# Kernel optimization log

Measured on AMD Instinct MI355X. Metric: run time of the kernel, lower is better.

## Reference

```python
import jax, jax.numpy as jnp
import numpy as np

HIDDEN = 1024

def setup_inputs() -> dict:
    key = jax.random.key(0)
    ks = jax.random.split(key, 7)
    s = 1.0 / np.sqrt(HIDDEN)
    X = jax.random.normal(ks[0], (4, 2048, HIDDEN), dtype=jnp.float32)
    Wq = jax.random.uniform(ks[1], (HIDDEN, HIDDEN), jnp.float32, -s, s)
    bq = jax.random.uniform(ks[2], (HIDDEN,), jnp.float32, -s, s)
    Wk = jax.random.uniform(ks[3], (HIDDEN, HIDDEN), jnp.float32, -s, s)
    bk = jax.random.uniform(ks[4], (HIDDEN,), jnp.float32, -s, s)
    Wv = jax.random.uniform(ks[5], (HIDDEN, HIDDEN), jnp.float32, -s, s)
    bv = jax.random.uniform(ks[6], (HIDDEN,), jnp.float32, -s, s)
    return {"X": X, "Wq": Wq, "bq": bq, "Wk": Wk, "bk": bk, "Wv": Wv, "bv": bv}

def reference(X, Wq, bq, Wk, bk, Wv, bv):
    # torch Linear: x @ W.T + b
    q = jnp.einsum('bsd,ed->bse', X, Wq) + bq  # [B,S,H]
    k = jnp.einsum('bsd,ed->bse', X, Wk) + bk
    v = jnp.einsum('bsd,ed->bse', X, Wv) + bv
    scores = jnp.einsum('bqd,bkd->bqk', q, k) / jnp.sqrt(jnp.float32(HIDDEN))  # [B,S,S]
    attn = jax.nn.softmax(scores, axis=-1)
    return jnp.einsum('bqk,bkd->bqd', attn, v)
```

## Files before the change

### kernel.cpp

```cpp
#include <hip/hip_runtime.h>
#include <hip/hip_bf16.h>
#include <stdint.h>

#define B_ 4
#define S_ 2048
#define H_ 1024

typedef __attribute__((ext_vector_type(4))) float f32x4;
typedef __attribute__((ext_vector_type(8))) short bf16x8;

#define AS1C(p) ((const __attribute__((address_space(1))) void*)(p))
#define AS3(p)  ((__attribute__((address_space(3))) void*)(p))

__global__ __launch_bounds__(256)
void prep_k(const float* __restrict__ X,
            const float* __restrict__ Wq, const float* __restrict__ Wk,
            const float* __restrict__ Wv,
            const float* __restrict__ bq, const float* __restrict__ bk,
            const float* __restrict__ bv,
            __hip_bfloat16* __restrict__ Xb, __hip_bfloat16* __restrict__ Wall,
            float* __restrict__ ball, float* __restrict__ rsum)
{
    const int NX = B_ * S_ * H_ / 4;
    const int NW = H_ * H_ / 4;
    int i = blockIdx.x * blockDim.x + threadIdx.x;
    if (i < NX + 3 * NW) {
        const float* src; uint64_t* dst; int li;
        if (i < NX) { src = X; dst = (uint64_t*)Xb; li = i; }
        else {
            int j = i - NX;
            int wsel = j / NW; li = j - wsel * NW;
            src = (wsel == 0) ? Wq : (wsel == 1) ? Wk : Wv;
            dst = (uint64_t*)Wall + (size_t)wsel * NW;
        }
        float4 v = ((const float4*)src)[li];
        union { __hip_bfloat16 h[4]; uint64_t u; } o;
        o.h[0] = __float2bfloat16(v.x);
        o.h[1] = __float2bfloat16(v.y);
        o.h[2] = __float2bfloat16(v.z);
        o.h[3] = __float2bfloat16(v.w);
        dst[li] = o.u;
    } else {
        int j = i - (NX + 3 * NW);
        if (j < 3 * H_ / 4) {
            int bsel = j >> 8;
            int off  = j & 255;
            const float* src = (bsel == 0) ? bq : (bsel == 1) ? bk : bv;
            ((float4*)ball)[j] = ((const float4*)src)[off];
        } else if (j < 3 * H_ / 4 + B_ * S_ / 4) {
            int j2 = j - 3 * H_ / 4;
            ((float4*)rsum)[j2] = make_float4(0.f, 0.f, 0.f, 0.f);
        }
    }
}

template<int BN, bool OUT_BF16, bool EXP_SUM, bool ROWDIV>
__global__ __launch_bounds__(512, 2)
void gemm2ph(const __hip_bfloat16* __restrict__ A, int lda, long long aBatch,
             const __hip_bfloat16* __restrict__ B, int ldb, long long bBatch,
             void* __restrict__ Cout, int ldc, long long cBatch,
             float* __restrict__ rsum, int K, float scale)
{
    constexpr int FJ = BN / 64;
    constexpr int GB = BN / 64;
    __shared__ __hip_bfloat16 lA[2 * 256 * 64];
    __shared__ __hip_bfloat16 lB[2 * BN * 64];

    const int t  = threadIdx.x;
    const int bz = blockIdx.z;
    A += (long long)bz * aBatch;
    B += (long long)bz * bBatch;
    const int bm = blockIdx.y * 256;
    const int bn = blockIdx.x * BN;

    const int wave = t >> 6;
    const int lane = t & 63;
    const int wm = (wave >> 2) * 128;
    const int wn = (wave & 3) * (BN / 4);
    const int lm = lane & 15;
    const int kq = lane >> 4;
    const int cro = lm & 7;

    const int srow = t >> 3;
    const int swz  = ((t & 7) ^ (srow & 7)) * 8;
    const __hip_bfloat16* gA = A + (long long)(bm + srow) * lda + swz;
    const __hip_bfloat16* gB = B + (long long)(bn + srow) * ldb + swz;

    f32x4 acc[8][FJ] = {};

    auto stage = [&](int buf, int k0) {
        __hip_bfloat16* dA = lA + buf * (256 * 64) + t * 8;
        __hip_bfloat16* dB = lB + buf * (BN * 64) + t * 8;
#pragma unroll
        for (int g = 0; g < 4; ++g)
            __builtin_amdgcn_global_load_lds(AS1C(gA + (long long)g * 64 * lda + k0),
                                             AS3(dA + g * 4096), 16, 0, 0);
#pragma unroll
        for (int g = 0; g < GB; ++g)
            __builtin_amdgcn_global_load_lds(AS1C(gB + (long long)g * 64 * ldb + k0),
                                             AS3(dB + g * 4096), 16, 0, 0);
    };

    stage(0, 0);
    __syncthreads();

    const int nT = K >> 6;
    int buf = 0;
    for (int tt = 0; tt < nT; ++tt) {
        if (tt + 1 < nT) stage(buf ^ 1, (tt + 1) * 64);
        const __hip_bfloat16* cA = lA + buf * (256 * 64) + (wm + lm) * 64;
        const __hip_bfloat16* cB = lB + buf * (BN * 64) + (wn + lm) * 64;
#pragma unroll
        for (int ks = 0; ks < 2; ++ks) {
            const int ch = ((ks * 4 + kq) ^ cro) * 8;
            bf16x8 af[8], bfr[FJ];
#pragma unroll
            for (int i = 0; i < 8; ++i)
                af[i] = *(const bf16x8*)(cA + i * 16 * 64 + ch);
#pragma unroll
            for (int j = 0; j < FJ; ++j)
                bfr[j] = *(const bf16x8*)(cB + j * 16 * 64 + ch);
#pragma unroll
            for (int i = 0; i < 8; ++i)
#pragma unroll
                for (int j = 0; j < FJ; ++j)
                    acc[i][j] = __builtin_amdgcn_mfma_f32_16x16x32_bf16(
                        af[i], bfr[j], acc[i][j], 0, 0, 0);
        }
        __syncthreads();
        buf ^= 1;
    }

    if (EXP_SUM) {
#pragma unroll
        for (int fi = 0; fi < 8; ++fi) {
            const int rowb = bm + wm + fi * 16 + kq * 4;
            float ps[4] = {0.f, 0.f, 0.f, 0.f};
#pragma unroll
            for (int nj = 0; nj < FJ; ++nj) {
                const int col = bn + wn + nj * 16 + lm;
#pragma unroll
                for (int r = 0; r < 4; ++r) {
                    float e = __expf(acc[fi][nj][r] * scale);
                    ps[r] += e;
                    ((__hip_bfloat16*)Cout)[(long long)bz * cBatch +
                        (long long)(rowb + r) * ldc + col] = __float2bfloat16(e);
                }
            }
#pragma unroll
            for (int r = 0; r < 4; ++r) {
#pragma unroll
                for (int m = 1; m < 16; m <<= 1)
                    ps[r] += __shfl_xor(ps[r], m);
            }
            if (lm == 0) {
#pragma unroll
                for (int r = 0; r < 4; ++r)
                    atomicAdd(rsum + bz * S_ + rowb + r, ps[r]);
            }
        }
        return;
    }

#pragma unroll
    for (int fi = 0; fi < 8; ++fi) {
        const int rowb = bm + wm + fi * 16 + kq * 4;
        float inv[4];
        if (ROWDIV) {
            float4 rs = *(const float4*)(rsum + bz * S_ + rowb);
            inv[0] = 1.0f / rs.x; inv[1] = 1.0f / rs.y;
            inv[2] = 1.0f / rs.z; inv[3] = 1.0f / rs.w;
        }
#pragma unroll
        for (int nj = 0; nj < FJ; ++nj) {
            const int col = bn + wn + nj * 16 + lm;
#pragma unroll
            for (int r = 0; r < 4; ++r) {
                float val = ROWDIV ? acc[fi][nj][r] * inv[r] : acc[fi][nj][r] * scale;
                long long idx = (long long)bz * cBatch + (long long)(rowb + r) * ldc + col;
                if (OUT_BF16) ((__hip_bfloat16*)Cout)[idx] = __float2bfloat16(val);
                else          ((float*)Cout)[idx] = val;
            }
        }
    }
}

template<int BN, int MINW, bool OUT_BF16, bool HAS_BIAS, bool V_SPLIT, bool EXP_SUM, bool ROWDIV>
__global__ __launch_bounds__(256, MINW)
void gemm_bt(const __hip_bfloat16* __restrict__ A, int lda, long long aBatch,
             const __hip_bfloat16* __restrict__ B, int ldb, long long bBatch,
             const float* __restrict__ bias,
             void* __restrict__ Cout, int ldc, long long cBatch,
             __hip_bfloat16* __restrict__ vtrans, float* __restrict__ rsum,
             int M, int N, int K, float scale)
{
    constexpr int FJ = BN / 32;
    constexpr int SN = BN / 32;
    __shared__ __hip_bfloat16 lA[128 * 64];
    __shared__ __hip_bfloat16 lB[BN * 64];

    const int t  = threadIdx.x;
    const int bz = blockIdx.z;
    A += (long long)bz * aBatch;
    B += (long long)bz * bBatch;
    const int bm = blockIdx.y * 128;
    const int bn = blockIdx.x * BN;

    const int wave = t >> 6;
    const int lane = t & 63;
    const int wm = (wave & 1) * 64;
    const int wn = (wave >> 1) * (BN / 2);
    const int lm = lane & 15;
    const int kq = lane >> 4;
    const int cro = lm & 7;

    f32x4 acc[4][FJ] = {};

    const int srow = t >> 3;
    const int swz  = ((t & 7) ^ ((t >> 3) & 7)) * 8;
    const __hip_bfloat16* gA = A + (long long)(bm + srow) * lda + swz;
    const __hip_bfloat16* gB = B + (long long)(bn + srow) * ldb + swz;
    __hip_bfloat16* sA = lA + t * 8;
    __hip_bfloat16* sB = lB + t * 8;

    for (int k0 = 0; k0 < K; k0 += 64) {
        __syncthreads();
#pragma unroll
        for (int s = 0; s < 4; ++s)
            __builtin_amdgcn_global_load_lds(AS1C(gA + (long long)s * 32 * lda + k0),
                                             AS3(sA + s * 2048), 16, 0, 0);
#pragma unroll
        for (int s = 0; s < SN; ++s)
            __builtin_amdgcn_global_load_lds(AS1C(gB + (long long)s * 32 * ldb + k0),
                                             AS3(sB + s * 2048), 16, 0, 0);
        __syncthreads();

#pragma unroll
        for (int ks = 0; ks < 2; ++ks) {
            bf16x8 af[4], bfr[FJ];
            const int ch = ((ks * 4 + kq) ^ cro) * 8;
#pragma unroll
            for (int i = 0; i < 4; ++i)
                af[i] = *(const bf16x8*)(lA + (wm + i * 16 + lm) * 64 + ch);
#pragma unroll
            for (int j = 0; j < FJ; ++j)
                bfr[j] = *(const bf16x8*)(lB + (wn + j * 16 + lm) * 64 + ch);
#pragma unroll
            for (int i = 0; i < 4; ++i)
#pragma unroll
                for (int j = 0; j < FJ; ++j)
                    acc[i][j] = __builtin_amdgcn_mfma_f32_16x16x32_bf16(af[i], bfr[j], acc[i][j], 0, 0, 0);
        }
    }

    const bool vmode = V_SPLIT && (bn >= 2 * H_);
    const int r0q = kq * 4;

    if (EXP_SUM) {
#pragma unroll
        for (int i = 0; i < 4; ++i) {
            const int rowb = bm + wm + i * 16 + r0q;
            float ps[4] = {0.f, 0.f, 0.f, 0.f};
#pragma unroll
            for (int j = 0; j < FJ; ++j) {
                const int col = bn + wn + j * 16 + lm;
#pragma unroll
                for (int r = 0; r < 4; ++r) {
                    float e = __expf(acc[i][j][r] * scale);
                    ps[r] += e;
                    ((__hip_bfloat16*)Cout)[(long long)bz * cBatch +
                        (long long)(rowb + r) * ldc + col] = __float2bfloat16(e);
                }
            }
#pragma unroll
            for (int r = 0; r < 4; ++r) {
#pragma unroll
                for (int m = 1; m < 16; m <<= 1)
                    ps[r] += __shfl_xor(ps[r], m);
            }
            if (lm == 0) {
#pragma unroll
                for (int r = 0; r < 4; ++r)
                    atomicAdd(rsum + bz * S_ + rowb + r, ps[r]);
            }
        }
        return;
    }

#pragma unroll
    for (int i = 0; i < 4; ++i) {
        const int rowb = bm + wm + i * 16 + r0q;
        float inv[4];
        if (ROWDIV) {
            float4 rs = *(const float4*)(rsum + bz * S_ + rowb);
            inv[0] = 1.0f / rs.x; inv[1] = 1.0f / rs.y;
            inv[2] = 1.0f / rs.z; inv[3] = 1.0f / rs.w;
        }
#pragma unroll
        for (int j = 0; j < FJ; ++j) {
            const int col = bn + wn + j * 16 + lm;
            float bvv = 0.0f;
            if (HAS_BIAS) bvv = bias[col];
            if (!vmode) {
#pragma unroll
                for (int r = 0; r < 4; ++r) {
                    float val = ROWDIV ? acc[i][j][r] * inv[r]
                                       : acc[i][j][r] * scale + bvv;
                    long long idx = (long long)bz * cBatch + (long long)(rowb + r) * ldc + col;
                    if (OUT_BF16) ((__hip_bfloat16*)Cout)[idx] = __float2bfloat16(val);
                    else          ((float*)Cout)[idx] = val;
                }
            } else {
                const long long ebase = (long long)((rowb >> 11) * H_ + col - 2 * H_) * S_;
                union { ushort4 u; __hip_bfloat16 h[4]; } o;
#pragma unroll
                for (int r = 0; r < 4; ++r)
                    o.h[r] = __float2bfloat16(acc[i][j][r] + bvv);
                *(ushort4*)(vtrans + ebase + (rowb & 2047)) = o.u;
            }
        }
    }
}

extern "C" void kernel_launch(void* const* d_in, const int* in_sizes, int n_in,
                              void* d_out, int out_size, void* d_ws, size_t ws_size,
                              hipStream_t stream)
{
    const float* X  = (const float*)d_in[0];
    const float* Wq = (const float*)d_in[1];
    const float* bq = (const float*)d_in[2];
    const float* Wk = (const float*)d_in[3];
    const float* bk = (const float*)d_in[4];
    const float* Wv = (const float*)d_in[5];
    const float* bv = (const float*)d_in[6];
    float* out = (float*)d_out;

    char* w = (char*)d_ws;
    const size_t MB = 1ull << 20;
    __hip_bfloat16* Xb   = (__hip_bfloat16*)(w + 0);
    __hip_bfloat16* Wall = (__hip_bfloat16*)(w + 16 * MB);
    float*          ball = (float*)        (w + 22 * MB);
    __hip_bfloat16* sc   = (__hip_bfloat16*)(w + 0);
    __hip_bfloat16* qk   = (__hip_bfloat16*)(w + 32 * MB);
    __hip_bfloat16* vtb  = (__hip_bfloat16*)(w + 64 * MB);
    float*          rsum = (float*)        (w + 80 * MB);

    const int prep_items = B_ * S_ * H_ / 4 + 3 * H_ * H_ / 4 + 3 * H_ / 4 + B_ * S_ / 4;
    prep_k<<<(prep_items + 255) / 256, 256, 0, stream>>>(X, Wq, Wk, Wv, bq, bk, bv,
                                                         Xb, Wall, ball, rsum);

    dim3 g1(3 * H_ / 128, (B_ * S_) / 128, 1);
    gemm_bt<128, 1, true, true, true, false, false><<<g1, 256, 0, stream>>>(
        Xb, H_, 0, Wall, H_, 0, ball, qk, 2 * H_, 0, vtb, nullptr,
        B_ * S_, 3 * H_, H_, 1.0f);

    dim3 g2(S_ / 256, S_ / 256, B_);
    gemm2ph<256, true, true, false><<<g2, 512, 0, stream>>>(
        qk,      2 * H_, (long long)S_ * 2 * H_,
        qk + H_, 2 * H_, (long long)S_ * 2 * H_,
        sc, S_, (long long)S_ * S_, rsum, H_, 0.03125f);

    dim3 g3(H_ / 128, S_ / 256, B_);
    gemm2ph<128, false, false, true><<<g3, 512, 0, stream>>>(
        sc,  S_, (long long)S_ * S_,
        vtb, S_, (long long)H_ * S_,
        out, H_, (long long)S_ * H_, rsum, S_, 1.0f);
}
```

Before: 253.0 us.

## Replace two-phase GEMM with 8-phase ping-pong pipelined 256x256 tile kernel

Replaces the double-buffered gemm2ph kernel with gemm8p, which splits each 64-wide K step into four quadrant sub-steps. Barriers, sched_barriers, explicit vmcnt waits and s_setprio interleave LDS fragment loads, async global-to-LDS staging and MFMA bursts. The PV GEMM moves from 256x128 to 256x256 tiles at one block per CU, which halves its grid, and the prep kernel becomes a grid-stride loop with a fixed 2048-block launch. The aim is better overlap of memory and MFMA, at the cost of many more barriers and lower occupancy.

```diff
diff --git a/kernel.cpp b/kernel.cpp
--- a/kernel.cpp
+++ b/kernel.cpp
@@ -11,6 +11,9 @@
 
 #define AS1C(p) ((const __attribute__((address_space(1))) void*)(p))
 #define AS3(p)  ((__attribute__((address_space(3))) void*)(p))
+#define BAR()     __builtin_amdgcn_s_barrier()
+#define SCHED0()  __builtin_amdgcn_sched_barrier(0)
+#define WAITVM(n) asm volatile("s_waitcnt vmcnt(" #n ")" ::: "memory")
 
 __global__ __launch_bounds__(256)
 void prep_k(const float* __restrict__ X,
@@ -23,125 +26,160 @@
 {
     const int NX = B_ * S_ * H_ / 4;
     const int NW = H_ * H_ / 4;
-    int i = blockIdx.x * blockDim.x + threadIdx.x;
-    if (i < NX + 3 * NW) {
-        const float* src; uint64_t* dst; int li;
-        if (i < NX) { src = X; dst = (uint64_t*)Xb; li = i; }
-        else {
-            int j = i - NX;
-            int wsel = j / NW; li = j - wsel * NW;
-            src = (wsel == 0) ? Wq : (wsel == 1) ? Wk : Wv;
-            dst = (uint64_t*)Wall + (size_t)wsel * NW;
-        }
-        float4 v = ((const float4*)src)[li];
-        union { __hip_bfloat16 h[4]; uint64_t u; } o;
-        o.h[0] = __float2bfloat16(v.x);
-        o.h[1] = __float2bfloat16(v.y);
-        o.h[2] = __float2bfloat16(v.z);
-        o.h[3] = __float2bfloat16(v.w);
-        dst[li] = o.u;
-    } else {
-        int j = i - (NX + 3 * NW);
-        if (j < 3 * H_ / 4) {
-            int bsel = j >> 8;
-            int off  = j & 255;
-            const float* src = (bsel == 0) ? bq : (bsel == 1) ? bk : bv;
-            ((float4*)ball)[j] = ((const float4*)src)[off];
-        } else if (j < 3 * H_ / 4 + B_ * S_ / 4) {
-            int j2 = j - 3 * H_ / 4;
-            ((float4*)rsum)[j2] = make_float4(0.f, 0.f, 0.f, 0.f);
+    const int TOT = NX + 3 * NW + 3 * H_ / 4 + B_ * S_ / 4;
+    const int stride = gridDim.x * blockDim.x;
+    for (int i = blockIdx.x * blockDim.x + threadIdx.x; i < TOT; i += stride) {
+        if (i < NX + 3 * NW) {
+            const float* src; uint64_t* dst; int li;
+            if (i < NX) { src = X; dst = (uint64_t*)Xb; li = i; }
+            else {
+                int j = i - NX;
+                int wsel = j / NW; li = j - wsel * NW;
+                src = (wsel == 0) ? Wq : (wsel == 1) ? Wk : Wv;
+                dst = (uint64_t*)Wall + (size_t)wsel * NW;
+            }
+            float4 v = ((const float4*)src)[li];
+            union { __hip_bfloat16 h[4]; uint64_t u; } o;
+            o.h[0] = __float2bfloat16(v.x);
+            o.h[1] = __float2bfloat16(v.y);
+            o.h[2] = __float2bfloat16(v.z);
+            o.h[3] = __float2bfloat16(v.w);
+            dst[li] = o.u;
+        } else {
+            int j = i - (NX + 3 * NW);
+            if (j < 3 * H_ / 4) {
+                int bsel = j >> 8;
+                int off  = j & 255;
+                const float* src = (bsel == 0) ? bq : (bsel == 1) ? bk : bv;
+                ((float4*)ball)[j] = ((const float4*)src)[off];
+            } else {
+                int j2 = j - 3 * H_ / 4;
+                ((float4*)rsum)[j2] = make_float4(0.f, 0.f, 0.f, 0.f);
+            }
         }
     }
 }
 
-template<int BN, bool OUT_BF16, bool EXP_SUM, bool ROWDIV>
-__global__ __launch_bounds__(512, 2)
-void gemm2ph(const __hip_bfloat16* __restrict__ A, int lda, long long aBatch,
-             const __hip_bfloat16* __restrict__ B, int ldb, long long bBatch,
-             void* __restrict__ Cout, int ldc, long long cBatch,
-             float* __restrict__ rsum, int K, float scale)
+template<bool EXP_SUM, bool ROWDIV, bool OUT_BF16>
+__global__ __launch_bounds__(512, 1)
+void gemm8p(const __hip_bfloat16* __restrict__ A, int lda, long long aBatch,
+            const __hip_bfloat16* __restrict__ B, int ldb, long long bBatch,
+            void* __restrict__ Cout, int ldc, long long cBatch,
+            float* __restrict__ rsum, int K, float scale)
 {
-    constexpr int FJ = BN / 64;
-    constexpr int GB = BN / 64;
-    __shared__ __hip_bfloat16 lA[2 * 256 * 64];
-    __shared__ __hip_bfloat16 lB[2 * BN * 64];
+    __shared__ __hip_bfloat16 lA[2][2][128 * 64];
+    __shared__ __hip_bfloat16 lB[2][2][128 * 64];
 
     const int t  = threadIdx.x;
     const int bz = blockIdx.z;
     A += (long long)bz * aBatch;
     B += (long long)bz * bBatch;
     const int bm = blockIdx.y * 256;
-    const int bn = blockIdx.x * BN;
-
-    const int wave = t >> 6;
-    const int lane = t & 63;
-    const int wm = (wave >> 2) * 128;
-    const int wn = (wave & 3) * (BN / 4);
-    const int lm = lane & 15;
-    const int kq = lane >> 4;
+    const int bn = blockIdx.x * 256;
+
+    const int wave = t >> 6, lane = t & 63;
+    const int wm2 = (wave >> 2) * 64;
+    const int wn2 = (wave & 3) * 32;
+    const int lm = lane & 15, kq = lane >> 4;
     const int cro = lm & 7;
 
+    f32x4 acc[8][4] = {};
+
     const int srow = t >> 3;
-    const int swz  = ((t & 7) ^ (srow & 7)) * 8;
-    const __hip_bfloat16* gA = A + (long long)(bm + srow) * lda + swz;
-    const __hip_bfloat16* gB = B + (long long)(bn + srow) * ldb + swz;
-
-    f32x4 acc[8][FJ] = {};
-
-    auto stage = [&](int buf, int k0) {
-        __hip_bfloat16* dA = lA + buf * (256 * 64) + t * 8;
-        __hip_bfloat16* dB = lB + buf * (BN * 64) + t * 8;
-#pragma unroll
-        for (int g = 0; g < 4; ++g)
-            __builtin_amdgcn_global_load_lds(AS1C(gA + (long long)g * 64 * lda + k0),
-                                             AS3(dA + g * 4096), 16, 0, 0);
-#pragma unroll
-        for (int g = 0; g < GB; ++g)
-            __builtin_amdgcn_global_load_lds(AS1C(gB + (long long)g * 64 * ldb + k0),
-                                             AS3(dB + g * 4096), 16, 0, 0);
+    const int sch  = (t & 7) ^ (srow & 7);
+    const __hip_bfloat16* gA = A + (long long)(bm + srow) * lda + sch * 8;
+    const __hip_bfloat16* gB = B + (long long)(bn + srow) * ldb + sch * 8;
+
+    auto stA = [&](int kt, int h) {
+        const __hip_bfloat16* s = gA + (long long)(h * 128) * lda + kt * 64;
+        __hip_bfloat16* d = &lA[kt & 1][h][t * 8];
+        __builtin_amdgcn_global_load_lds(AS1C(s), AS3(d), 16, 0, 0);
+        __builtin_amdgcn_global_load_lds(AS1C(s + (long long)64 * lda), AS3(d + 4096), 16, 0, 0);
     };
-
-    stage(0, 0);
-    __syncthreads();
-
-    const int nT = K >> 6;
-    int buf = 0;
-    for (int tt = 0; tt < nT; ++tt) {
-        if (tt + 1 < nT) stage(buf ^ 1, (tt + 1) * 64);
-        const __hip_bfloat16* cA = lA + buf * (256 * 64) + (wm + lm) * 64;
-        const __hip_bfloat16* cB = lB + buf * (BN * 64) + (wn + lm) * 64;
-#pragma unroll
-        for (int ks = 0; ks < 2; ++ks) {
-            const int ch = ((ks * 4 + kq) ^ cro) * 8;
-            bf16x8 af[8], bfr[FJ];
-#pragma unroll
-            for (int i = 0; i < 8; ++i)
-                af[i] = *(const bf16x8*)(cA + i * 16 * 64 + ch);
-#pragma unroll
-            for (int j = 0; j < FJ; ++j)
-                bfr[j] = *(const bf16x8*)(cB + j * 16 * 64 + ch);
-#pragma unroll
-            for (int i = 0; i < 8; ++i)
-#pragma unroll
-                for (int j = 0; j < FJ; ++j)
-                    acc[i][j] = __builtin_amdgcn_mfma_f32_16x16x32_bf16(
-                        af[i], bfr[j], acc[i][j], 0, 0, 0);
-        }
-        __syncthreads();
-        buf ^= 1;
+    auto stB = [&](int kt, int h) {
+        const __hip_bfloat16* s = gB + (long long)(h * 128) * ldb + kt * 64;
+        __hip_bfloat16* d = &lB[kt & 1][h][t * 8];
+        __builtin_amdgcn_global_load_lds(AS1C(s), AS3(d), 16, 0, 0);
+        __builtin_amdgcn_global_load_lds(AS1C(s + (long long)64 * ldb), AS3(d + 4096), 16, 0, 0);
+    };
+
+    bf16x8 af[2][4], bfr[2][2];
+    auto ldA = [&](int d, int h) {
+#pragma unroll
+        for (int ks = 0; ks < 2; ++ks)
+#pragma unroll
+            for (int fi = 0; fi < 4; ++fi)
+                af[ks][fi] = *(const bf16x8*)&lA[d][h][(wm2 + fi * 16 + lm) * 64 +
+                                                       (((ks * 4 + kq) ^ cro) * 8)];
+    };
+    auto ldB = [&](int d, int h) {
+#pragma unroll
+        for (int ks = 0; ks < 2; ++ks)
+#pragma unroll
+            for (int nj = 0; nj < 2; ++nj)
+                bfr[ks][nj] = *(const bf16x8*)&lB[d][h][(wn2 + nj * 16 + lm) * 64 +
+                                                        (((ks * 4 + kq) ^ cro) * 8)];
+    };
+    auto mm = [&](int Mh, int Nh) {
+        __builtin_amdgcn_s_setprio(1);
+#pragma unroll
+        for (int ks = 0; ks < 2; ++ks)
+#pragma unroll
+            for (int fi = 0; fi < 4; ++fi)
+#pragma unroll
+                for (int nj = 0; nj < 2; ++nj)
+                    acc[Mh * 4 + fi][Nh * 2 + nj] = __builtin_amdgcn_mfma_f32_16x16x32_bf16(
+                        af[ks][fi], bfr[ks][nj], acc[Mh * 4 + fi][Nh * 2 + nj], 0, 0, 0);
+        __builtin_amdgcn_s_setprio(0);
+    };
+
+    const int nkt = K >> 6;
+    stA(0, 0); stA(0, 1); stB(0, 0); stB(0, 1);
+    stA(1, 0); stA(1, 1);
+    SCHED0(); WAITVM(4); SCHED0(); BAR(); SCHED0();
+
+    for (int kt = 0; kt < nkt; ++kt) {
+        const int d = kt & 1;
+        ldA(d, 0); ldB(d, 0);
+        if (kt + 1 < nkt) { stB(kt + 1, 0); stB(kt + 1, 1); }
+        BAR(); SCHED0();
+        mm(0, 0);
+        BAR(); SCHED0();
+        ldB(d, 1);
+        if (kt + 2 < nkt) stA(kt + 2, 0);
+        BAR(); SCHED0();
+        mm(0, 1);
+        BAR(); SCHED0();
+        ldA(d, 1); ldB(d, 0);
+        BAR(); SCHED0();
+        mm(1, 0);
+        BAR(); SCHED0();
+        ldB(d, 1);
+        if (kt + 2 < nkt) stA(kt + 2, 1);
+        BAR(); SCHED0();
+        mm(1, 1);
+        if (kt + 1 < nkt) {
+            if (kt + 2 < nkt) { WAITVM(4); } else { WAITVM(0); }
+        }
+        SCHED0();
+        BAR(); SCHED0();
     }
 
     if (EXP_SUM) {
 #pragma unroll
-        for (int fi = 0; fi < 8; ++fi) {
-            const int rowb = bm + wm + fi * 16 + kq * 4;
+        for (int Mh = 0; Mh < 2; ++Mh)
+#pragma unroll
+        for (int fi = 0; fi < 4; ++fi) {
+            const int rowb = bm + Mh * 128 + wm2 + fi * 16 + kq * 4;
             float ps[4] = {0.f, 0.f, 0.f, 0.f};
 #pragma unroll
-            for (int nj = 0; nj < FJ; ++nj) {
-                const int col = bn + wn + nj * 16 + lm;
+            for (int Nh = 0; Nh < 2; ++Nh)
+#pragma unroll
+            for (int nj = 0; nj < 2; ++nj) {
+                const int col = bn + Nh * 128 + wn2 + nj * 16 + lm;
 #pragma unroll
                 for (int r = 0; r < 4; ++r) {
-                    float e = __expf(acc[fi][nj][r] * scale);
+                    float e = __expf(acc[Mh * 4 + fi][Nh * 2 + nj][r] * scale);
                     ps[r] += e;
                     ((__hip_bfloat16*)Cout)[(long long)bz * cBatch +
                         (long long)(rowb + r) * ldc + col] = __float2bfloat16(e);
@@ -163,8 +201,10 @@
     }
 
 #pragma unroll
-    for (int fi = 0; fi < 8; ++fi) {
-        const int rowb = bm + wm + fi * 16 + kq * 4;
+    for (int Mh = 0; Mh < 2; ++Mh)
+#pragma unroll
+    for (int fi = 0; fi < 4; ++fi) {
+        const int rowb = bm + Mh * 128 + wm2 + fi * 16 + kq * 4;
         float inv[4];
         if (ROWDIV) {
             float4 rs = *(const float4*)(rsum + bz * S_ + rowb);
@@ -172,11 +212,14 @@
             inv[2] = 1.0f / rs.z; inv[3] = 1.0f / rs.w;
         }
 #pragma unroll
-        for (int nj = 0; nj < FJ; ++nj) {
-            const int col = bn + wn + nj * 16 + lm;
+        for (int Nh = 0; Nh < 2; ++Nh)
+#pragma unroll
+        for (int nj = 0; nj < 2; ++nj) {
+            const int col = bn + Nh * 128 + wn2 + nj * 16 + lm;
 #pragma unroll
             for (int r = 0; r < 4; ++r) {
-                float val = ROWDIV ? acc[fi][nj][r] * inv[r] : acc[fi][nj][r] * scale;
+                float val = ROWDIV ? acc[Mh * 4 + fi][Nh * 2 + nj][r] * inv[r]
+                                   : acc[Mh * 4 + fi][Nh * 2 + nj][r] * scale;
                 long long idx = (long long)bz * cBatch + (long long)(rowb + r) * ldc + col;
                 if (OUT_BF16) ((__hip_bfloat16*)Cout)[idx] = __float2bfloat16(val);
                 else          ((float*)Cout)[idx] = val;
@@ -345,9 +388,8 @@
     __hip_bfloat16* vtb  = (__hip_bfloat16*)(w + 64 * MB);
     float*          rsum = (float*)        (w + 80 * MB);
 
-    const int prep_items = B_ * S_ * H_ / 4 + 3 * H_ * H_ / 4 + 3 * H_ / 4 + B_ * S_ / 4;
-    prep_k<<<(prep_items + 255) / 256, 256, 0, stream>>>(X, Wq, Wk, Wv, bq, bk, bv,
-                                                         Xb, Wall, ball, rsum);
+    prep_k<<<2048, 256, 0, stream>>>(X, Wq, Wk, Wv, bq, bk, bv,
+                                     Xb, Wall, ball, rsum);
 
     dim3 g1(3 * H_ / 128, (B_ * S_) / 128, 1);
     gemm_bt<128, 1, true, true, true, false, false><<<g1, 256, 0, stream>>>(
@@ -355,13 +397,13 @@
         B_ * S_, 3 * H_, H_, 1.0f);
 
     dim3 g2(S_ / 256, S_ / 256, B_);
-    gemm2ph<256, true, true, false><<<g2, 512, 0, stream>>>(
+    gemm8p<true, false, true><<<g2, 512, 0, stream>>>(
         qk,      2 * H_, (long long)S_ * 2 * H_,
         qk + H_, 2 * H_, (long long)S_ * 2 * H_,
         sc, S_, (long long)S_ * S_, rsum, H_, 0.03125f);
 
-    dim3 g3(H_ / 128, S_ / 256, B_);
-    gemm2ph<128, false, false, true><<<g3, 512, 0, stream>>>(
+    dim3 g3(H_ / 256, S_ / 256, B_);
+    gemm8p<false, true, false><<<g3, 512, 0, stream>>>(
         sc,  S_, (long long)S_ * S_,
         vtb, S_, (long long)H_ * S_,
         out, H_, (long long)S_ * H_, rsum, S_, 1.0f);
```

New measurement: 267.1 us. +5.6%, slower.
